# Kernel tuning notes

Measured on AMD Instinct MI355X. Metric: run time of the kernel, lower is better.

Reference implementation:

```python
import jax, jax.numpy as jnp
import numpy as np
from jax import lax

# dims
BATCH, SEQ, DMODEL = 2, 2048, 1024
EXPAND, HEADDIM, DSTATE, DCONV, MLP_INNER = 2, 64, 64, 4, 4096
DIN = EXPAND * DMODEL            # 2048
NH = DIN // HEADDIM              # 32 heads
CONV_DIM = DIN + 2 * DSTATE      # x, B, C go through the depthwise conv
DPROJ = 2 * DIN + 2 * DSTATE + NH  # z, xBC, dt
EPS = 1e-5


def rmsnorm(x, w):
    return x * lax.rsqrt(jnp.mean(x * x, axis=-1, keepdims=True) + EPS) * w


def setup_inputs() -> dict:
    key = jax.random.key(0)
    ks = jax.random.split(key, 12)
    n = lambda i, shape, scale: jax.random.normal(ks[i], shape, jnp.float32) * scale
    return {
        "hidden_tokens": n(0, (BATCH, SEQ, DMODEL), 1.0),
        "W_in": n(1, (DMODEL, DPROJ), DMODEL ** -0.5),
        "conv_w": n(2, (CONV_DIM, DCONV), 0.2),
        "conv_b": jnp.zeros((CONV_DIM,), jnp.float32),
        "dt_bias": jax.random.uniform(ks[3], (NH,), jnp.float32, -4.0, -1.0),
        "A_log": jnp.log(jax.random.uniform(ks[4], (NH,), jnp.float32, 1.0, 16.0)),
        "D_param": n(5, (NH,), 1.0),
        "norm_w": jnp.ones((DIN,), jnp.float32),
        "W_out": n(6, (DIN, DMODEL), DIN ** -0.5),
        "rms_w": jnp.ones((DMODEL,), jnp.float32),
        "mlp_w1": n(7, (DMODEL, MLP_INNER), DMODEL ** -0.5),
        "mlp_b1": jnp.zeros((MLP_INNER,), jnp.float32),
        "mlp_w2": n(8, (MLP_INNER, DMODEL), MLP_INNER ** -0.5),
        "mlp_b2": jnp.zeros((DMODEL,), jnp.float32),
    }


def _mamba2(x, W_in, conv_w, conv_b, dt_bias, A_log, D_param, norm_w, W_out):
    b, l, _ = x.shape
    zxbcdt = x @ W_in                                   # (b,l,DPROJ)
    z = zxbcdt[..., :DIN]
    xBC = zxbcdt[..., DIN:DIN + CONV_DIM]
    dt = zxbcdt[..., DIN + CONV_DIM:]                   # (b,l,NH)

    # depthwise causal conv1d over sequence
    xt = jnp.pad(xBC, ((0, 0), (DCONV - 1, 0), (0, 0))).transpose(0, 2, 1)  # (b,c,l+pad)
    conv = lax.conv_general_dilated(xt, conv_w[:, None, :], (1,), "VALID",
                                    feature_group_count=CONV_DIM,
                                    dimension_numbers=("NCH", "OIH", "NCH"))
    xBC = jax.nn.silu(conv.transpose(0, 2, 1) + conv_b)  # (b,l,CONV_DIM)

    xs = xBC[..., :DIN].reshape(b, l, NH, HEADDIM)       # (b,l,h,p)
    Bc = xBC[..., DIN:DIN + DSTATE]                      # (b,l,n), ngroups=1
    Cc = xBC[..., DIN + DSTATE:]                         # (b,l,n)

    dt = jax.nn.softplus(dt + dt_bias)                   # (b,l,h)
    A = -jnp.exp(A_log)                                  # (h,)
    dA = jnp.exp(dt * A)                                 # (b,l,h)
    dtx = dt[..., None] * xs                             # (b,l,h,p)

    def step(h, inp):
        dA_t, dtx_t, B_t, C_t = inp                      # (b,h),(b,h,p),(b,n),(b,n)
        h = dA_t[..., None, None] * h + dtx_t[..., None] * B_t[:, None, None, :]
        y = jnp.einsum("bhpn,bn->bhp", h, C_t)
        return h, y

    h0 = jnp.zeros((b, NH, HEADDIM, DSTATE), x.dtype)
    _, ys = lax.scan(step, h0, (dA.transpose(1, 0, 2), dtx.transpose(1, 0, 2, 3),
                                Bc.transpose(1, 0, 2), Cc.transpose(1, 0, 2)))
    y = ys.transpose(1, 0, 2, 3) + D_param[None, None, :, None] * xs  # (b,l,h,p)
    y = y.reshape(b, l, DIN)
    y = rmsnorm(y * jax.nn.silu(z), norm_w)              # gated RMSNorm
    return y @ W_out


def reference(hidden_tokens, W_in, conv_w, conv_b, dt_bias, A_log, D_param,
              norm_w, W_out, rms_w, mlp_w1, mlp_b1, mlp_w2, mlp_b2):
    h = hidden_tokens + _mamba2(hidden_tokens, W_in, conv_w, conv_b, dt_bias,
                                A_log, D_param, norm_w, W_out)
    hn = rmsnorm(h, rms_w)
    mlp = jax.nn.silu(hn @ mlp_w1 + mlp_b1) @ mlp_w2 + mlp_b2
    return h + mlp
```

## Files before the change

kernel.cpp:

```cpp
#include <hip/hip_runtime.h>
#include <hip/hip_bf16.h>
#include <cstdint>
#include <cstddef>

#define BATCH 2
#define SEQ 2048
#define DMODEL 1024
#define DIN 2048
#define NH 32
#define HEADDIM 64
#define DSTATE 64
#define DCONV 4
#define CONV_DIM (DIN + 2 * DSTATE)
#define DPROJ (2 * DIN + 2 * DSTATE + NH)
#define MLP_INNER 4096
#define TOKENS (BATCH * SEQ)
#define EPS 1e-5f
#define Q 64
#define NCHUNK (SEQ / Q)
#define NCH (BATCH * NCHUNK * NH)
#define LSTR 72
#define NPAD_IN 4352

typedef __attribute__((ext_vector_type(8))) short short8;
typedef __attribute__((ext_vector_type(8))) __bf16 bf16x8;
typedef __attribute__((ext_vector_type(4))) float f32x4;

__device__ inline short f2bf(float f) {
    unsigned u = __builtin_bit_cast(unsigned, f);
    u = (u + 0x7FFFu + ((u >> 16) & 1u)) >> 16;
    return (short)u;
}
__device__ inline float bf2f(short s) {
    unsigned u = ((unsigned)(unsigned short)s) << 16;
    return __builtin_bit_cast(float, u);
}
__device__ inline float silu_f(float x) { return x / (1.f + __expf(-x)); }

__device__ inline bf16x8 ld_frag(const short* p) {
    short8 s = *(const short8*)p;
    return __builtin_bit_cast(bf16x8, s);
}

__device__ inline void glds16(const short* g, short* l) {
    __builtin_amdgcn_global_load_lds(
        (const __attribute__((address_space(1))) void*)g,
        (__attribute__((address_space(3))) void*)l, 16, 0, 0);
}

template <int MODE>
__global__ __launch_bounds__(512, 4) void gemm_bf16_kernel(
    const short* __restrict__ A, const short* __restrict__ BT,
    void* __restrict__ Cout, const float* __restrict__ bias,
    int M, int N, int K)
{
    constexpr int KT = 64;
    const int tid  = threadIdx.x;
    const int wid  = tid >> 6;
    const int lane = tid & 63;
    const int lm   = lane & 15;
    const int lg   = lane >> 4;
    const int wm   = (wid >> 2) * 64;
    const int wn   = (wid & 3) * 32;

    const int nb  = gridDim.x * gridDim.y;
    const int bid = blockIdx.y * gridDim.x + blockIdx.x;
    const int per = nb >> 3;
    const int nid = (bid & 7) * per + (bid >> 3);
    const int m0  = (nid / gridDim.x) * 128;
    const int n0  = (nid % gridDim.x) * 128;

    __shared__ __attribute__((aligned(16))) short Al0[128 * KT];
    __shared__ __attribute__((aligned(16))) short Al1[128 * KT];
    __shared__ __attribute__((aligned(16))) short Bl0[128 * KT];
    __shared__ __attribute__((aligned(16))) short Bl1[128 * KT];

    f32x4 acc[4][2];
#pragma unroll
    for (int i = 0; i < 4; ++i)
#pragma unroll
        for (int j = 0; j < 2; ++j) acc[i][j] = {0.f, 0.f, 0.f, 0.f};

    const int srow = lane >> 3;
    const int scb  = (lane & 7) ^ srow;
    const short* Ag = A  + (size_t)(m0 + wid * 16 + srow) * K + scb * 8;
    const short* Bg = BT + (size_t)(n0 + wid * 16 + srow) * K + scb * 8;
    const int woff = wid * 16 * KT;

    const int niter = K / KT;
    {
#pragma unroll
        for (int j = 0; j < 2; ++j) {
            glds16(Ag + (size_t)j * 8 * K, Al0 + woff + j * 512);
            glds16(Bg + (size_t)j * 8 * K, Bl0 + woff + j * 512);
        }
    }

    for (int i = 0; i < niter; ++i) {
        __syncthreads();
        const short* Ac = (i & 1) ? Al1 : Al0;
        const short* Bc = (i & 1) ? Bl1 : Bl0;
        if (i + 1 < niter) {
            int kt = (i + 1) * KT;
            short* al = ((i & 1) ? Al0 : Al1) + woff;
            short* bl = ((i & 1) ? Bl0 : Bl1) + woff;
#pragma unroll
            for (int j = 0; j < 2; ++j) {
                glds16(Ag + kt + (size_t)j * 8 * K, al + j * 512);
                glds16(Bg + kt + (size_t)j * 8 * K, bl + j * 512);
            }
        }

#pragma unroll
        for (int sub = 0; sub < 2; ++sub) {
            const int cb = sub * 4 + lg;
            bf16x8 af[4], bf[2];
#pragma unroll
            for (int ii = 0; ii < 4; ++ii) {
                int ar = wm + ii * 16 + lm;
                af[ii] = ld_frag(&Ac[ar * KT + ((cb ^ (ar & 7)) * 8)]);
            }
#pragma unroll
            for (int j = 0; j < 2; ++j) {
                int br = wn + j * 16 + lm;
                bf[j] = ld_frag(&Bc[br * KT + ((cb ^ (br & 7)) * 8)]);
            }
#pragma unroll
            for (int ii = 0; ii < 4; ++ii)
#pragma unroll
                for (int j = 0; j < 2; ++j)
                    acc[ii][j] = __builtin_amdgcn_mfma_f32_16x16x32_bf16(af[ii], bf[j], acc[ii][j], 0, 0, 0);
        }
    }

#pragma unroll
    for (int j = 0; j < 2; ++j) {
        int col = n0 + wn + j * 16 + lm;
        if (col >= N) continue;
        float bv = (MODE == 1) ? bias[col] : 0.f;
#pragma unroll
        for (int i = 0; i < 4; ++i) {
#pragma unroll
            for (int r = 0; r < 4; ++r) {
                int row = m0 + wm + i * 16 + lg * 4 + r;
                float v = acc[i][j][r];
                if (MODE == 1) v = silu_f(v + bv);
                ((short*)Cout)[(size_t)row * N + col] = f2bf(v);
            }
        }
    }
}

template <int MODE>
__global__ __launch_bounds__(512, 4) void gemm64_kernel(
    const short* __restrict__ A, const short* __restrict__ BT,
    void* __restrict__ Cout, const float* __restrict__ bias,
    const float* __restrict__ res, int M, int N, int K)
{
    constexpr int KT = 64;
    const int tid  = threadIdx.x;
    const int wid  = tid >> 6;
    const int lane = tid & 63;
    const int lm   = lane & 15;
    const int lg   = lane >> 4;
    const int wm   = (wid >> 2) * 32;
    const int wn   = (wid & 3) * 32;

    const int nb  = gridDim.x * gridDim.y;
    const int bid = blockIdx.y * gridDim.x + blockIdx.x;
    const int per = nb >> 3;
    const int nid = (bid & 7) * per + (bid >> 3);
    const int m0  = (nid / gridDim.x) * 64;
    const int n0  = (nid % gridDim.x) * 128;

    __shared__ __attribute__((aligned(16))) short Al0[64 * KT];
    __shared__ __attribute__((aligned(16))) short Al1[64 * KT];
    __shared__ __attribute__((aligned(16))) short Bl0[128 * KT];
    __shared__ __attribute__((aligned(16))) short Bl1[128 * KT];

    f32x4 acc[2][2];
#pragma unroll
    for (int i = 0; i < 2; ++i)
#pragma unroll
        for (int j = 0; j < 2; ++j) acc[i][j] = {0.f, 0.f, 0.f, 0.f};

    const int srow = lane >> 3;
    const int scb  = (lane & 7) ^ srow;
    const short* Bg = BT + (size_t)(n0 + wid * 16 + srow) * K + scb * 8;
    const short* Ag = A  + (size_t)(m0 + (wid & 3) * 16 + srow) * K + scb * 8;
    const int woffB = wid * 16 * KT;
    const int woffA = (wid & 3) * 16 * KT;
    const bool doA = (wid < 4);

    const int niter = K / KT;
    {
#pragma unroll
        for (int j = 0; j < 2; ++j) {
            if (doA) glds16(Ag + (size_t)j * 8 * K, Al0 + woffA + j * 512);
            glds16(Bg + (size_t)j * 8 * K, Bl0 + woffB + j * 512);
        }
    }

    for (int i = 0; i < niter; ++i) {
        __syncthreads();
        const short* Ac = (i & 1) ? Al1 : Al0;
        const short* Bc = (i & 1) ? Bl1 : Bl0;
        if (i + 1 < niter) {
            int kt = (i + 1) * KT;
            short* al = ((i & 1) ? Al0 : Al1) + woffA;
            short* bl = ((i & 1) ? Bl0 : Bl1) + woffB;
#pragma unroll
            for (int j = 0; j < 2; ++j) {
                if (doA) glds16(Ag + kt + (size_t)j * 8 * K, al + j * 512);
                glds16(Bg + kt + (size_t)j * 8 * K, bl + j * 512);
            }
        }

#pragma unroll
        for (int sub = 0; sub < 2; ++sub) {
            const int cb = sub * 4 + lg;
            bf16x8 af[2], bf[2];
#pragma unroll
            for (int ii = 0; ii < 2; ++ii) {
                int ar = wm + ii * 16 + lm;
                af[ii] = ld_frag(&Ac[ar * KT + ((cb ^ (ar & 7)) * 8)]);
            }
#pragma unroll
            for (int j = 0; j < 2; ++j) {
                int br = wn + j * 16 + lm;
                bf[j] = ld_frag(&Bc[br * KT + ((cb ^ (br & 7)) * 8)]);
            }
#pragma unroll
            for (int ii = 0; ii < 2; ++ii)
#pragma unroll
                for (int j = 0; j < 2; ++j)
                    acc[ii][j] = __builtin_amdgcn_mfma_f32_16x16x32_bf16(af[ii], bf[j], acc[ii][j], 0, 0, 0);
        }
    }

#pragma unroll
    for (int j = 0; j < 2; ++j) {
        int col = n0 + wn + j * 16 + lm;
        float bv = (MODE == 2) ? bias[col] : 0.f;
#pragma unroll
        for (int i = 0; i < 2; ++i) {
#pragma unroll
            for (int r = 0; r < 4; ++r) {
                int row = m0 + wm + i * 16 + lg * 4 + r;
                float v = acc[i][j][r] + bv + res[(size_t)row * N + col];
                ((float*)Cout)[(size_t)row * N + col] = v;
            }
        }
    }
}

__global__ __launch_bounds__(256) void cvt_kernel(
    const float* __restrict__ src, short* __restrict__ dst, int n4)
{
    int i = (blockIdx.x * 256 + threadIdx.x);
    if (i >= n4) return;
    f32x4 v = *(const f32x4*)(src + (size_t)i * 4);
    short4 o;
    o.x = f2bf(v.x); o.y = f2bf(v.y); o.z = f2bf(v.z); o.w = f2bf(v.w);
    *(short4*)(dst + (size_t)i * 4) = o;
}

__global__ __launch_bounds__(256) void transpose_kernel(
    const float* __restrict__ src, short* __restrict__ dst, int K, int N)
{
    __shared__ float t[32][33];
    int bx = blockIdx.x, by = blockIdx.y;
    int col = threadIdx.x & 31, row8 = threadIdx.x >> 5;
    int gn = bx * 32 + col;
#pragma unroll
    for (int r = 0; r < 4; ++r) {
        int gk = by * 32 + row8 + r * 8;
        t[row8 + r * 8][col] = (gn < N) ? src[(size_t)gk * N + gn] : 0.f;
    }
    __syncthreads();
#pragma unroll
    for (int r = 0; r < 4; ++r) {
        int n = bx * 32 + row8 + r * 8;
        dst[(size_t)n * K + by * 32 + col] = f2bf(t[col][row8 + r * 8]);
    }
}

#define CTOK 8
__global__ __launch_bounds__(256) void conv_kernel(
    const short* __restrict__ zx, const float* __restrict__ cw,
    const float* __restrict__ cb, short* __restrict__ xBCc)
{
    int c4 = blockIdx.y * 256 + threadIdx.x;
    if (c4 >= CONV_DIM / 4) return;
    int c  = c4 * 4;
    int m0 = blockIdx.x * CTOK;
    int l0 = m0 & (SEQ - 1);

    const short* base = zx + (size_t)m0 * DPROJ + DIN + c;
    f32x4 win[CTOK + 3];
#pragma unroll
    for (int j = 0; j < CTOK + 3; ++j) {
        int off = j - 3;
        if (l0 + off >= 0) {
            short4 sv = *(const short4*)(base + (ptrdiff_t)off * DPROJ);
            win[j] = {bf2f(sv.x), bf2f(sv.y), bf2f(sv.z), bf2f(sv.w)};
        } else {
            win[j] = {0.f, 0.f, 0.f, 0.f};
        }
    }
    f32x4 w0 = *(const f32x4*)(cw + (c + 0) * DCONV);
    f32x4 w1 = *(const f32x4*)(cw + (c + 1) * DCONV);
    f32x4 w2 = *(const f32x4*)(cw + (c + 2) * DCONV);
    f32x4 w3 = *(const f32x4*)(cw + (c + 3) * DCONV);
    f32x4 bb = *(const f32x4*)(cb + c);

    short* outp = xBCc + (size_t)m0 * CONV_DIM + c;
#pragma unroll
    for (int t = 0; t < CTOK; ++t) {
        f32x4 a = {bb.x, bb.y, bb.z, bb.w};
#pragma unroll
        for (int j = 0; j < DCONV; ++j) {
            f32x4 v = win[t + j];
            a.x += v.x * w0[j];
            a.y += v.y * w1[j];
            a.z += v.z * w2[j];
            a.w += v.w * w3[j];
        }
        short4 o;
        o.x = f2bf(silu_f(a.x)); o.y = f2bf(silu_f(a.y));
        o.z = f2bf(silu_f(a.z)); o.w = f2bf(silu_f(a.w));
        *(short4*)(outp + (size_t)t * CONV_DIM) = o;
    }
}

__global__ __launch_bounds__(256) void dt_kernel(
    const short* __restrict__ zx, const float* __restrict__ dt_bias,
    const float* __restrict__ A_log, float* __restrict__ dtb, float* __restrict__ ldab)
{
    int idx = blockIdx.x * 256 + threadIdx.x;
    if (idx >= TOKENS * NH) return;
    int hh = idx & (NH - 1);
    int m  = idx >> 5;
    float v  = bf2f(zx[(size_t)m * DPROJ + DIN + CONV_DIM + hh]) + dt_bias[hh];
    float dt = (v > 20.f) ? v : log1pf(__expf(v));
    dtb[idx]  = dt;
    ldab[idx] = -__expf(A_log[hh]) * dt;
}

__global__ __launch_bounds__(256) void chunk_kernel(
    const short* __restrict__ xBCc, const float* __restrict__ dtb,
    const float* __restrict__ ldab, short* __restrict__ ybuf,
    short* __restrict__ Sbuf, float* __restrict__ cumdecay)
{
    int bid = blockIdx.x;
    int h = bid & 31, c = (bid >> 5) & 31, b = bid >> 10;
    int m0 = b * SEQ + c * Q;
    int tid = threadIdx.x;
    int wid = tid >> 6, lane = tid & 63, lm = lane & 15, lg = lane >> 4;

    __shared__ __attribute__((aligned(16))) short Cc[64 * LSTR];
    __shared__ __attribute__((aligned(16))) short Bb[64 * LSTR];
    __shared__ __attribute__((aligned(16))) short BwT[64 * LSTR];
    __shared__ __attribute__((aligned(16))) short Xt[64 * LSTR];
    __shared__ __attribute__((aligned(16))) short Mm[64 * LSTR];
    __shared__ float Lc[64], dtv[64];

    if (tid < 64) {
        int s = tid;
        size_t ix = (size_t)(m0 + s) * NH + h;
        float ld = ldab[ix];
        float dt = dtb[ix];
        float v = ld;
#pragma unroll
        for (int off = 1; off < 64; off <<= 1) {
            float o = __shfl_up(v, off);
            if (s >= off) v += o;
        }
        Lc[s] = v;
        dtv[s] = dt;
        cumdecay[(size_t)bid * 64 + s] = __expf(v);
    }
    {
        int row = tid >> 2, c0 = (tid & 3) * 16;
        const short* pB = xBCc + (size_t)(m0 + row) * CONV_DIM + DIN;
#pragma unroll
        for (int u = 0; u < 2; ++u) {
            short8 vb = *(const short8*)(pB + c0 + 8 * u);
            short8 vc = *(const short8*)(pB + DSTATE + c0 + 8 * u);
            *(short8*)&Bb[row * LSTR + c0 + 8 * u] = vb;
            *(short8*)&Cc[row * LSTR + c0 + 8 * u] = vc;
        }
    }
    __syncthreads();
    {
        int s = tid >> 2, c0 = (tid & 3) * 16;
        float w = dtv[s];
        float w2 = __expf(Lc[63] - Lc[s]);
        const short* pX = xBCc + (size_t)(m0 + s) * CONV_DIM + h * HEADDIM;
#pragma unroll
        for (int u = 0; u < 4; ++u) {
            short4 v = *(const short4*)(pX + c0 + 4 * u);
            Xt[(c0 + 4 * u + 0) * LSTR + s] = f2bf(bf2f(v.x) * w);
            Xt[(c0 + 4 * u + 1) * LSTR + s] = f2bf(bf2f(v.y) * w);
            Xt[(c0 + 4 * u + 2) * LSTR + s] = f2bf(bf2f(v.z) * w);
            Xt[(c0 + 4 * u + 3) * LSTR + s] = f2bf(bf2f(v.w) * w);
            short4 sb = *(short4*)&Bb[s * LSTR + c0 + 4 * u];
            BwT[(c0 + 4 * u + 0) * LSTR + s] = f2bf(bf2f(sb.x) * w2);
            BwT[(c0 + 4 * u + 1) * LSTR + s] = f2bf(bf2f(sb.y) * w2);
            BwT[(c0 + 4 * u + 2) * LSTR + s] = f2bf(bf2f(sb.z) * w2);
            BwT[(c0 + 4 * u + 3) * LSTR + s] = f2bf(bf2f(sb.w) * w2);
        }
    }
    __syncthreads();

    {
        bf16x8 af[2];
#pragma unroll
        for (int kk = 0; kk < 2; ++kk)
            af[kk] = ld_frag(&Cc[(wid * 16 + lm) * LSTR + kk * 32 + lg * 8]);
#pragma unroll
        for (int j = 0; j < 4; ++j) {
            f32x4 acc = {0.f, 0.f, 0.f, 0.f};
#pragma unroll
            for (int kk = 0; kk < 2; ++kk) {
                bf16x8 bf = ld_frag(&Bb[(j * 16 + lm) * LSTR + kk * 32 + lg * 8]);
                acc = __builtin_amdgcn_mfma_f32_16x16x32_bf16(af[kk], bf, acc, 0, 0, 0);
            }
            int s = j * 16 + lm;
            float Ls = Lc[s];
#pragma unroll
            for (int r = 0; r < 4; ++r) {
                int t = wid * 16 + lg * 4 + r;
                float val = (s <= t) ? acc[r] * __expf(Lc[t] - Ls) : 0.f;
                Mm[t * LSTR + s] = f2bf(val);
            }
        }
    }
    __syncthreads();

    {
        bf16x8 am[2], aw[2];
#pragma unroll
        for (int kk = 0; kk < 2; ++kk) {
            am[kk] = ld_frag(&Mm[(wid * 16 + lm) * LSTR + kk * 32 + lg * 8]);
            aw[kk] = ld_frag(&BwT[(wid * 16 + lm) * LSTR + kk * 32 + lg * 8]);
        }
#pragma unroll
        for (int j = 0; j < 4; ++j) {
            f32x4 a1 = {0.f, 0.f, 0.f, 0.f};
            f32x4 a2 = {0.f, 0.f, 0.f, 0.f};
#pragma unroll
            for (int kk = 0; kk < 2; ++kk) {
                bf16x8 bx = ld_frag(&Xt[(j * 16 + lm) * LSTR + kk * 32 + lg * 8]);
                a1 = __builtin_amdgcn_mfma_f32_16x16x32_bf16(am[kk], bx, a1, 0, 0, 0);
                a2 = __builtin_amdgcn_mfma_f32_16x16x32_bf16(aw[kk], bx, a2, 0, 0, 0);
            }
            int p = j * 16 + lm;
#pragma unroll
            for (int r = 0; r < 4; ++r) {
                int t = wid * 16 + lg * 4 + r;
                ybuf[(size_t)(m0 + t) * DIN + h * HEADDIM + p] = f2bf(a1[r]);
                Sbuf[(size_t)bid * 4096 + t * 64 + p] = f2bf(a2[r]);
            }
        }
    }
}

__global__ __launch_bounds__(256) void state_kernel(
    short* __restrict__ SH, const float* __restrict__ cumdecay)
{
    int bh = blockIdx.x >> 2, st = blockIdx.x & 3;
    int b = bh >> 5, h = bh & 31;
    int off = st * 1024 + threadIdx.x * 4;

    f32x4 H = {0.f, 0.f, 0.f, 0.f};
    int cid = b * NCHUNK * NH + h;
    short4 sv = *(const short4*)(SH + (size_t)cid * 4096 + off);
    float cd_next = cumdecay[(size_t)cid * 64 + 63];

    for (int c = 0; c < NCHUNK; ++c) {
        short4 s4 = sv;
        float cd = cd_next;
        size_t base = (size_t)cid * 4096 + off;
        if (c + 1 < NCHUNK) {
            sv = *(const short4*)(SH + base + (size_t)NH * 4096);
            cd_next = cumdecay[(size_t)(cid + NH) * 64 + 63];
        }
        short4 o;
        o.x = f2bf(H.x); o.y = f2bf(H.y); o.z = f2bf(H.z); o.w = f2bf(H.w);
        *(short4*)(SH + base) = o;
        H.x = cd * H.x + bf2f(s4.x);
        H.y = cd * H.y + bf2f(s4.y);
        H.z = cd * H.z + bf2f(s4.z);
        H.w = cd * H.w + bf2f(s4.w);
        cid += NH;
    }
}

__global__ __launch_bounds__(256) void inter_kernel(
    const short* __restrict__ xBCc, const short* __restrict__ Hin,
    const float* __restrict__ cumdecay, short* __restrict__ ybuf)
{
    int bid = blockIdx.x;
    int h = bid & 31, c = (bid >> 5) & 31, b = bid >> 10;
    int m0 = b * SEQ + c * Q;
    int tid = threadIdx.x;
    int wid = tid >> 6, lane = tid & 63, lm = lane & 15, lg = lane >> 4;

    __shared__ __attribute__((aligned(16))) short Cc[64 * LSTR];
    __shared__ __attribute__((aligned(16))) short HT[64 * LSTR];
    __shared__ float eLc[64];

    if (tid < 64) eLc[tid] = cumdecay[(size_t)bid * 64 + tid];
    {
        int row = tid >> 2, c0 = (tid & 3) * 16;
        const short* pC = xBCc + (size_t)(m0 + row) * CONV_DIM + DIN + DSTATE;
#pragma unroll
        for (int u = 0; u < 2; ++u) {
            short8 vc = *(const short8*)(pC + c0 + 8 * u);
            *(short8*)&Cc[row * LSTR + c0 + 8 * u] = vc;
        }
        const short* pH = Hin + (size_t)bid * 4096 + row * 64;
        short8 h0 = *(const short8*)(pH + c0);
        short8 h1 = *(const short8*)(pH + c0 + 8);
#pragma unroll
        for (int u = 0; u < 8; ++u) {
            HT[(c0 + u) * LSTR + row]     = h0[u];
            HT[(c0 + 8 + u) * LSTR + row] = h1[u];
        }
    }
    __syncthreads();

    bf16x8 af[2];
#pragma unroll
    for (int kk = 0; kk < 2; ++kk)
        af[kk] = ld_frag(&Cc[(wid * 16 + lm) * LSTR + kk * 32 + lg * 8]);
#pragma unroll
    for (int j = 0; j < 4; ++j) {
        f32x4 acc = {0.f, 0.f, 0.f, 0.f};
#pragma unroll
        for (int kk = 0; kk < 2; ++kk) {
            bf16x8 bh_ = ld_frag(&HT[(j * 16 + lm) * LSTR + kk * 32 + lg * 8]);
            acc = __builtin_amdgcn_mfma_f32_16x16x32_bf16(af[kk], bh_, acc, 0, 0, 0);
        }
        int p = j * 16 + lm;
#pragma unroll
        for (int r = 0; r < 4; ++r) {
            int t = wid * 16 + lg * 4 + r;
            size_t ya = (size_t)(m0 + t) * DIN + h * HEADDIM + p;
            ybuf[ya] = f2bf(bf2f(ybuf[ya]) + eLc[t] * acc[r]);
        }
    }
}

__global__ __launch_bounds__(256) void norm1_kernel(
    const short* __restrict__ zx, const short* __restrict__ xBCc,
    const float* __restrict__ Dp, const short* __restrict__ y,
    short* __restrict__ ybf, const float* __restrict__ w)
{
    int m = blockIdx.x;
    int t = threadIdx.x;
    int i0 = t * 8;
    const short8 zv = *(const short8*)(zx + (size_t)m * DPROJ + i0);
    const short8 xv = *(const short8*)(xBCc + (size_t)m * CONV_DIM + i0);
    const short8 yv = *(const short8*)(y + (size_t)m * DIN + i0);
    float Dv = Dp[i0 >> 6];

    float vals[8];
    float ss = 0.f;
#pragma unroll
    for (int j = 0; j < 8; ++j) {
        float v = (bf2f(yv[j]) + Dv * bf2f(xv[j])) * silu_f(bf2f(zv[j]));
        vals[j] = v;
        ss += v * v;
    }
#pragma unroll
    for (int o = 32; o >= 1; o >>= 1) ss += __shfl_xor(ss, o);
    __shared__ float wsum[4];
    if ((t & 63) == 0) wsum[t >> 6] = ss;
    __syncthreads();
    float tot = wsum[0] + wsum[1] + wsum[2] + wsum[3];
    float scale = rsqrtf(tot / (float)DIN + EPS);

    f32x4 w0 = *(const f32x4*)(w + i0);
    f32x4 w1 = *(const f32x4*)(w + i0 + 4);
    short8 ov;
#pragma unroll
    for (int j = 0; j < 8; ++j) {
        float wj = (j < 4) ? w0[j] : w1[j - 4];
        ov[j] = f2bf(vals[j] * scale * wj);
    }
    *(short8*)(ybf + (size_t)m * DIN + i0) = ov;
}

__global__ __launch_bounds__(256) void norm2_kernel(
    const float* __restrict__ hb, short* __restrict__ hnbf, const float* __restrict__ w)
{
    int m = blockIdx.x;
    int t = threadIdx.x;
    int i0 = t * 4;
    f32x4 hv = *(const f32x4*)(hb + (size_t)m * DMODEL + i0);
    float ss = hv.x * hv.x + hv.y * hv.y + hv.z * hv.z + hv.w * hv.w;
#pragma unroll
    for (int o = 32; o >= 1; o >>= 1) ss += __shfl_xor(ss, o);
    __shared__ float wsum[4];
    if ((t & 63) == 0) wsum[t >> 6] = ss;
    __syncthreads();
    float tot = wsum[0] + wsum[1] + wsum[2] + wsum[3];
    float scale = rsqrtf(tot / (float)DMODEL + EPS);
    f32x4 wv = *(const f32x4*)(w + i0);
    short4 ov;
    ov.x = f2bf(hv.x * scale * wv.x);
    ov.y = f2bf(hv.y * scale * wv.y);
    ov.z = f2bf(hv.z * scale * wv.z);
    ov.w = f2bf(hv.w * scale * wv.w);
    *(short4*)(hnbf + (size_t)m * DMODEL + i0) = ov;
}

extern "C" void kernel_launch(void* const* d_in, const int* in_sizes, int n_in,
                              void* d_out, int out_size, void* d_ws, size_t ws_size,
                              hipStream_t stream) {
    const float* x       = (const float*)d_in[0];
    const float* W_in    = (const float*)d_in[1];
    const float* conv_w  = (const float*)d_in[2];
    const float* conv_b  = (const float*)d_in[3];
    const float* dt_bias = (const float*)d_in[4];
    const float* A_log   = (const float*)d_in[5];
    const float* D_param = (const float*)d_in[6];
    const float* norm_w  = (const float*)d_in[7];
    const float* W_out   = (const float*)d_in[8];
    const float* rms_w   = (const float*)d_in[9];
    const float* mlp_w1  = (const float*)d_in[10];
    const float* mlp_b1  = (const float*)d_in[11];
    const float* mlp_w2  = (const float*)d_in[12];
    const float* mlp_b2  = (const float*)d_in[13];
    float* out = (float*)d_out;

    float* ws       = (float*)d_ws;
    float* zxf      = ws;
    float* xBCf     = zxf + (size_t)TOKENS * DPROJ;
    float* dtb      = xBCf + (size_t)TOKENS * CONV_DIM;
    float* ldab     = dtb + (size_t)TOKENS * NH;
    float* cumdecay = ldab + (size_t)TOKENS * NH;
    float* ybuf     = cumdecay + (size_t)TOKENS * NH;
    float* SH       = ybuf + (size_t)TOKENS * DIN;
    float* bfarea   = SH + (size_t)NCH * 4096;

    short* zxb   = (short*)zxf;
    short* xBCb  = (short*)xBCf;
    short* xbf   = (short*)ybuf;
    short* midbf = (short*)ybuf;
    short* ybufs = (short*)ybuf;
    short* SHs   = (short*)SH;
    float* hbuf  = SH;
    short* hnbf  = (short*)(SH + (size_t)TOKENS * DMODEL);

    short* ybf   = (short*)bfarea;
    short* WinT  = ybf + (size_t)TOKENS * DIN;
    short* WoutT = WinT + (size_t)NPAD_IN * DMODEL;
    short* w1T   = WoutT + (size_t)DMODEL * DIN;
    short* w2T   = w1T + (size_t)MLP_INNER * DMODEL;

    dim3 blk(256);
    dim3 blk2(512);

    cvt_kernel<<<dim3(TOKENS * DMODEL / 4 / 256), blk, 0, stream>>>(x, xbf, TOKENS * DMODEL / 4);
    transpose_kernel<<<dim3(NPAD_IN / 32, DMODEL / 32), blk, 0, stream>>>(W_in, WinT, DMODEL, DPROJ);
    transpose_kernel<<<dim3(DMODEL / 32, DIN / 32), blk, 0, stream>>>(W_out, WoutT, DIN, DMODEL);
    transpose_kernel<<<dim3(MLP_INNER / 32, DMODEL / 32), blk, 0, stream>>>(mlp_w1, w1T, DMODEL, MLP_INNER);
    transpose_kernel<<<dim3(DMODEL / 32, MLP_INNER / 32), blk, 0, stream>>>(mlp_w2, w2T, MLP_INNER, DMODEL);

    gemm_bf16_kernel<4><<<dim3(NPAD_IN / 128, TOKENS / 128), blk2, 0, stream>>>(
        xbf, WinT, zxb, nullptr, TOKENS, DPROJ, DMODEL);
    conv_kernel<<<dim3(TOKENS / CTOK, (CONV_DIM / 4 + 255) / 256), blk, 0, stream>>>(
        zxb, conv_w, conv_b, xBCb);
    dt_kernel<<<dim3(TOKENS * NH / 256), blk, 0, stream>>>(zxb, dt_bias, A_log, dtb, ldab);
    chunk_kernel<<<dim3(NCH), blk, 0, stream>>>(xBCb, dtb, ldab, ybufs, SHs, cumdecay);
    state_kernel<<<dim3(BATCH * NH * 4), blk, 0, stream>>>(SHs, cumdecay);
    inter_kernel<<<dim3(NCH), blk, 0, stream>>>(xBCb, SHs, cumdecay, ybufs);
    norm1_kernel<<<dim3(TOKENS), blk, 0, stream>>>(zxb, xBCb, D_param, ybufs, ybf, norm_w);
    gemm64_kernel<3><<<dim3(DMODEL / 128, TOKENS / 64), blk2, 0, stream>>>(
        ybf, WoutT, hbuf, nullptr, x, TOKENS, DMODEL, DIN);
    norm2_kernel<<<dim3(TOKENS), blk, 0, stream>>>(hbuf, hnbf, rms_w);
    gemm_bf16_kernel<1><<<dim3(MLP_INNER / 128, TOKENS / 128), blk2, 0, stream>>>(
        hnbf, w1T, midbf, mlp_b1, TOKENS, MLP_INNER, DMODEL);
    gemm64_kernel<2><<<dim3(DMODEL / 128, TOKENS / 64), blk2, 0, stream>>>(
        midbf, w2T, out, mlp_b2, hbuf, TOKENS, DMODEL, MLP_INNER);
}
```

Measured before the change: 393.5 us.

## Merge prep kernels, fold dt into conv, stage chunk/inter outputs through LDS

Merges the input conversion and the four weight transposes into one prep kernel, cutting four launches. The dt/softplus computation moves into the idle threads of the conv kernel's last y-block, so dt_kernel is gone. chunk_kernel and inter_kernel now stage their MFMA outputs in shared memory and write ybuf/Sbuf with coalesced 16-byte stores, replacing scattered 2-byte global stores. The cost is extra LDS traffic and barriers, plus branchy block dispatch in the prep kernel.

```diff
diff --git a/kernel.cpp b/kernel.cpp
--- a/kernel.cpp
+++ b/kernel.cpp
@@ -20,6 +20,7 @@
 #define NCHUNK (SEQ / Q)
 #define NCH (BATCH * NCHUNK * NH)
 #define LSTR 72
+#define BSTR 68
 #define NPAD_IN 4352
 
 typedef __attribute__((ext_vector_type(8))) short short8;
@@ -254,22 +255,34 @@
     }
 }
 
-__global__ __launch_bounds__(256) void cvt_kernel(
-    const float* __restrict__ src, short* __restrict__ dst, int n4)
-{
-    int i = (blockIdx.x * 256 + threadIdx.x);
-    if (i >= n4) return;
-    f32x4 v = *(const f32x4*)(src + (size_t)i * 4);
-    short4 o;
-    o.x = f2bf(v.x); o.y = f2bf(v.y); o.z = f2bf(v.z); o.w = f2bf(v.w);
-    *(short4*)(dst + (size_t)i * 4) = o;
-}
-
-__global__ __launch_bounds__(256) void transpose_kernel(
-    const float* __restrict__ src, short* __restrict__ dst, int K, int N)
-{
+#define PREP_CVT 4096
+#define PREP_T1  (PREP_CVT + 4352)
+#define PREP_T2  (PREP_T1 + 2048)
+#define PREP_T3  (PREP_T2 + 4096)
+#define PREP_T4  (PREP_T3 + 4096)
+__global__ __launch_bounds__(256) void prep_kernel(
+    const float* __restrict__ x, short* __restrict__ xbf,
+    const float* __restrict__ W_in, short* __restrict__ WinT,
+    const float* __restrict__ W_out, short* __restrict__ WoutT,
+    const float* __restrict__ w1, short* __restrict__ w1T,
+    const float* __restrict__ w2, short* __restrict__ w2T)
+{
+    int blk = blockIdx.x;
+    if (blk < PREP_CVT) {
+        int i = blk * 256 + threadIdx.x;
+        f32x4 v = *(const f32x4*)(x + (size_t)i * 4);
+        short4 o;
+        o.x = f2bf(v.x); o.y = f2bf(v.y); o.z = f2bf(v.z); o.w = f2bf(v.w);
+        *(short4*)(xbf + (size_t)i * 4) = o;
+        return;
+    }
     __shared__ float t[32][33];
-    int bx = blockIdx.x, by = blockIdx.y;
+    const float* src; short* dst; int K, N, bx, by;
+    if (blk < PREP_T1)      { int l = blk - PREP_CVT; bx = l % 136; by = l / 136; src = W_in;  dst = WinT;  K = DMODEL;    N = DPROJ; }
+    else if (blk < PREP_T2) { int l = blk - PREP_T1;  bx = l % 32;  by = l / 32;  src = W_out; dst = WoutT; K = DIN;       N = DMODEL; }
+    else if (blk < PREP_T3) { int l = blk - PREP_T2;  bx = l % 128; by = l / 128; src = w1;    dst = w1T;   K = DMODEL;    N = MLP_INNER; }
+    else                    { int l = blk - PREP_T3;  bx = l % 32;  by = l / 32;  src = w2;    dst = w2T;   K = MLP_INNER; N = DMODEL; }
+
     int col = threadIdx.x & 31, row8 = threadIdx.x >> 5;
     int gn = bx * 32 + col;
 #pragma unroll
@@ -288,12 +301,29 @@
 #define CTOK 8
 __global__ __launch_bounds__(256) void conv_kernel(
     const short* __restrict__ zx, const float* __restrict__ cw,
-    const float* __restrict__ cb, short* __restrict__ xBCc)
+    const float* __restrict__ cb, short* __restrict__ xBCc,
+    const float* __restrict__ dt_bias, const float* __restrict__ A_log,
+    float* __restrict__ dtb, float* __restrict__ ldab)
 {
     int c4 = blockIdx.y * 256 + threadIdx.x;
-    if (c4 >= CONV_DIM / 4) return;
+    int m0 = blockIdx.x * CTOK;
+    if (c4 >= CONV_DIM / 4) {
+        int i0 = (int)threadIdx.x - 32;
+#pragma unroll
+        for (int k = 0; k < 2; ++k) {
+            int i = i0 + k * 224;
+            if (i < 256) {
+                int hh = i & 31;
+                int m = m0 + (i >> 5);
+                float v = bf2f(zx[(size_t)m * DPROJ + DIN + CONV_DIM + hh]) + dt_bias[hh];
+                float dtv_ = (v > 20.f) ? v : log1pf(__expf(v));
+                dtb[(size_t)m0 * NH + i]  = dtv_;
+                ldab[(size_t)m0 * NH + i] = -__expf(A_log[hh]) * dtv_;
+            }
+        }
+        return;
+    }
     int c  = c4 * 4;
-    int m0 = blockIdx.x * CTOK;
     int l0 = m0 & (SEQ - 1);
 
     const short* base = zx + (size_t)m0 * DPROJ + DIN + c;
@@ -331,20 +361,6 @@
         o.z = f2bf(silu_f(a.z)); o.w = f2bf(silu_f(a.w));
         *(short4*)(outp + (size_t)t * CONV_DIM) = o;
     }
-}
-
-__global__ __launch_bounds__(256) void dt_kernel(
-    const short* __restrict__ zx, const float* __restrict__ dt_bias,
-    const float* __restrict__ A_log, float* __restrict__ dtb, float* __restrict__ ldab)
-{
-    int idx = blockIdx.x * 256 + threadIdx.x;
-    if (idx >= TOKENS * NH) return;
-    int hh = idx & (NH - 1);
-    int m  = idx >> 5;
-    float v  = bf2f(zx[(size_t)m * DPROJ + DIN + CONV_DIM + hh]) + dt_bias[hh];
-    float dt = (v > 20.f) ? v : log1pf(__expf(v));
-    dtb[idx]  = dt;
-    ldab[idx] = -__expf(A_log[hh]) * dt;
 }
 
 __global__ __launch_bounds__(256) void chunk_kernel(
@@ -459,10 +475,24 @@
 #pragma unroll
             for (int r = 0; r < 4; ++r) {
                 int t = wid * 16 + lg * 4 + r;
-                ybuf[(size_t)(m0 + t) * DIN + h * HEADDIM + p] = f2bf(a1[r]);
-                Sbuf[(size_t)bid * 4096 + t * 64 + p] = f2bf(a2[r]);
-            }
-        }
+                Cc[t * LSTR + p] = f2bf(a1[r]);
+                Bb[t * LSTR + p] = f2bf(a2[r]);
+            }
+        }
+    }
+    __syncthreads();
+    {
+        int row = tid >> 2, seg = (tid & 3) * 16;
+        short8 y0 = *(short8*)&Cc[row * LSTR + seg];
+        short8 y1 = *(short8*)&Cc[row * LSTR + seg + 8];
+        short* yb = ybuf + (size_t)(m0 + row) * DIN + h * HEADDIM + seg;
+        *(short8*)yb = y0;
+        *(short8*)(yb + 8) = y1;
+        short8 s0 = *(short8*)&Bb[row * LSTR + seg];
+        short8 s1 = *(short8*)&Bb[row * LSTR + seg + 8];
+        short* sb = Sbuf + (size_t)bid * 4096 + row * 64 + seg;
+        *(short8*)sb = s0;
+        *(short8*)(sb + 8) = s1;
     }
 }
 
@@ -507,8 +537,9 @@
     int tid = threadIdx.x;
     int wid = tid >> 6, lane = tid & 63, lm = lane & 15, lg = lane >> 4;
 
-    __shared__ __attribute__((aligned(16))) short Cc[64 * LSTR];
-    __shared__ __attribute__((aligned(16))) short HT[64 * LSTR];
+    __shared__ __attribute__((aligned(16))) short base_lds[2 * 64 * LSTR];
+    short* Cc = base_lds;
+    short* HT = base_lds + 64 * LSTR;
     __shared__ float eLc[64];
 
     if (tid < 64) eLc[tid] = cumdecay[(size_t)bid * 64 + tid];
@@ -535,6 +566,7 @@
 #pragma unroll
     for (int kk = 0; kk < 2; ++kk)
         af[kk] = ld_frag(&Cc[(wid * 16 + lm) * LSTR + kk * 32 + lg * 8]);
+    f32x4 accs[4];
 #pragma unroll
     for (int j = 0; j < 4; ++j) {
         f32x4 acc = {0.f, 0.f, 0.f, 0.f};
@@ -543,13 +575,42 @@
             bf16x8 bh_ = ld_frag(&HT[(j * 16 + lm) * LSTR + kk * 32 + lg * 8]);
             acc = __builtin_amdgcn_mfma_f32_16x16x32_bf16(af[kk], bh_, acc, 0, 0, 0);
         }
-        int p = j * 16 + lm;
-#pragma unroll
-        for (int r = 0; r < 4; ++r) {
-            int t = wid * 16 + lg * 4 + r;
-            size_t ya = (size_t)(m0 + t) * DIN + h * HEADDIM + p;
-            ybuf[ya] = f2bf(bf2f(ybuf[ya]) + eLc[t] * acc[r]);
-        }
+        accs[j] = acc;
+    }
+    __syncthreads();
+    {
+        float* bnc = (float*)base_lds;
+#pragma unroll
+        for (int j = 0; j < 4; ++j) {
+            int p = j * 16 + lm;
+#pragma unroll
+            for (int r = 0; r < 4; ++r) {
+                int t = wid * 16 + lg * 4 + r;
+                bnc[t * BSTR + p] = eLc[t] * accs[j][r];
+            }
+        }
+    }
+    __syncthreads();
+    {
+        float* bnc = (float*)base_lds;
+        int row = tid >> 2, seg = (tid & 3) * 16;
+        f32x4 b0 = *(f32x4*)&bnc[row * BSTR + seg];
+        f32x4 b1 = *(f32x4*)&bnc[row * BSTR + seg + 4];
+        f32x4 b2 = *(f32x4*)&bnc[row * BSTR + seg + 8];
+        f32x4 b3 = *(f32x4*)&bnc[row * BSTR + seg + 12];
+        short* yb = ybuf + (size_t)(m0 + row) * DIN + h * HEADDIM + seg;
+        short8 y0 = *(short8*)yb;
+        short8 y1 = *(short8*)(yb + 8);
+        short8 o0, o1;
+#pragma unroll
+        for (int u = 0; u < 4; ++u) {
+            o0[u]     = f2bf(bf2f(y0[u])     + b0[u]);
+            o0[u + 4] = f2bf(bf2f(y0[u + 4]) + b1[u]);
+            o1[u]     = f2bf(bf2f(y1[u])     + b2[u]);
+            o1[u + 4] = f2bf(bf2f(y1[u + 4]) + b3[u]);
+        }
+        *(short8*)yb = o0;
+        *(short8*)(yb + 8) = o1;
     }
 }
 
@@ -664,17 +725,13 @@
     dim3 blk(256);
     dim3 blk2(512);
 
-    cvt_kernel<<<dim3(TOKENS * DMODEL / 4 / 256), blk, 0, stream>>>(x, xbf, TOKENS * DMODEL / 4);
-    transpose_kernel<<<dim3(NPAD_IN / 32, DMODEL / 32), blk, 0, stream>>>(W_in, WinT, DMODEL, DPROJ);
-    transpose_kernel<<<dim3(DMODEL / 32, DIN / 32), blk, 0, stream>>>(W_out, WoutT, DIN, DMODEL);
-    transpose_kernel<<<dim3(MLP_INNER / 32, DMODEL / 32), blk, 0, stream>>>(mlp_w1, w1T, DMODEL, MLP_INNER);
-    transpose_kernel<<<dim3(DMODEL / 32, MLP_INNER / 32), blk, 0, stream>>>(mlp_w2, w2T, MLP_INNER, DMODEL);
+    prep_kernel<<<dim3(PREP_T4), blk, 0, stream>>>(
+        x, xbf, W_in, WinT, W_out, WoutT, mlp_w1, w1T, mlp_w2, w2T);
 
     gemm_bf16_kernel<4><<<dim3(NPAD_IN / 128, TOKENS / 128), blk2, 0, stream>>>(
         xbf, WinT, zxb, nullptr, TOKENS, DPROJ, DMODEL);
     conv_kernel<<<dim3(TOKENS / CTOK, (CONV_DIM / 4 + 255) / 256), blk, 0, stream>>>(
-        zxb, conv_w, conv_b, xBCb);
-    dt_kernel<<<dim3(TOKENS * NH / 256), blk, 0, stream>>>(zxb, dt_bias, A_log, dtb, ldab);
+        zxb, conv_w, conv_b, xBCb, dt_bias, A_log, dtb, ldab);
     chunk_kernel<<<dim3(NCH), blk, 0, stream>>>(xBCb, dtb, ldab, ybufs, SHs, cumdecay);
     state_kernel<<<dim3(BATCH * NH * 4), blk, 0, stream>>>(SHs, cumdecay);
     inter_kernel<<<dim3(NCH), blk, 0, stream>>>(xBCb, SHs, cumdecay, ybufs);
```

After: 363.5 us (median of 2 runs). 1.08x faster.
